# Performance work log

Hardware: AMD Instinct MI355X
Metric: run time of the kernel (lower is better)

## Reference

```python
import jax, jax.numpy as jnp
import numpy as np

C_IN = 64
C_QK = C_IN // 8  # 8
B, H, W = 8, 64, 64


def setup_inputs() -> dict:
    key = jax.random.key(0)
    ks = jax.random.split(key, 8)
    s_in = 1.0 / np.sqrt(C_IN)
    return {
        "x": jax.random.normal(ks[0], (B, C_IN, H, W), dtype=jnp.float32),
        "Wf": jax.random.normal(ks[1], (C_QK, C_IN), dtype=jnp.float32) * s_in,
        "bf": jax.random.normal(ks[2], (C_QK,), dtype=jnp.float32) * 0.01,
        "Wg": jax.random.normal(ks[3], (C_QK, C_IN), dtype=jnp.float32) * s_in,
        "bg": jax.random.normal(ks[4], (C_QK,), dtype=jnp.float32) * 0.01,
        "Wh": jax.random.normal(ks[5], (C_IN, C_IN), dtype=jnp.float32) * s_in,
        "bh": jax.random.normal(ks[6], (C_IN,), dtype=jnp.float32) * 0.01,
        "gamma": jax.random.normal(ks[7], (1,), dtype=jnp.float32) * 0.1,
    }


def reference(x, Wf, bf, Wg, bg, Wh, bh, gamma):
    Bn, C, Hn, Wn = x.shape
    N = Hn * Wn
    xf = x.reshape(Bn, C, N)  # (B, C, HW)
    # 1x1 convs == per-pixel linear projections
    fx = jnp.einsum('bcn,oc->bno', xf, Wf) + bf            # (B, HW, C/8)  (permuted query)
    gx = jnp.einsum('bcn,oc->bon', xf, Wg) + bg[:, None]   # (B, C/8, HW)
    hx = jnp.einsum('bcn,oc->bon', xf, Wh) + bh[:, None]   # (B, C,  HW)
    s_mtx = jnp.einsum('bno,bom->bnm', fx, gx)             # (B, HW, HW)
    attention = jax.nn.softmax(s_mtx, axis=-2)             # softmax over dim=-2 (rows)
    o = jnp.einsum('bcn,bnm->bcm', hx, attention)          # (B, C, HW)
    return x + gamma * o.reshape(Bn, C, Hn, Wn)
```

## Files before the change

kernel.cpp:

```cpp
#include <hip/hip_runtime.h>
#include <hip/hip_bf16.h>
#include <math.h>

#define CIN 64
#define CQK 8
#define BATCH 8
#define NPOS 4096
#define TN 128
#define NT (NPOS / TN)

typedef __attribute__((ext_vector_type(8))) short s16x8;
typedef __attribute__((ext_vector_type(4))) float f32x4;
typedef __attribute__((ext_vector_type(16))) float f32x16;

#define Z16 {0,0,0,0,0,0,0,0,0,0,0,0,0,0,0,0}

#define SCH_BIAS 1065353216.0f

__device__ inline unsigned cvt_pk_bf16(float lo, float hi) {
    unsigned r;
    asm("v_cvt_pk_bf16_f32 %0, %1, %2" : "=v"(r) : "v"(lo), "v"(hi));
    return r;
}
__device__ inline float sch_exp(float y) {
    return __builtin_bit_cast(float, (int)y);
}

__global__ __launch_bounds__(256) void proj_kernel(
    const float* __restrict__ x,
    const float* __restrict__ Wf, const float* __restrict__ bf,
    const float* __restrict__ Wg, const float* __restrict__ bg,
    const float* __restrict__ Wh, const float* __restrict__ bh,
    unsigned short* __restrict__ Kp, unsigned short* __restrict__ Qp,
    unsigned short* __restrict__ Vimg)
{
    __shared__ float xs[CIN * 34];
    __shared__ float bss[80];

    const int tid = threadIdx.x;
    const int b   = blockIdx.y;
    const int n0  = blockIdx.x * 32;

    if (tid < 80)
        bss[tid] = (tid < 8) ? bf[tid] : (tid < 16) ? bg[tid - 8] : bh[tid - 16];

    {
        const int c   = tid >> 2;
        const int seg = tid & 3;
        const float* src = x + ((size_t)(b * CIN + c)) * NPOS + n0 + seg * 8;
        float* dst = xs + c * 34 + seg * 8;
#pragma unroll
        for (int k = 0; k < 2; ++k) {
            const float4 v = *(const float4*)(src + k * 4);
            *(float2*)(dst + k * 4)     = make_float2(v.x, v.y);
            *(float2*)(dst + k * 4 + 2) = make_float2(v.z, v.w);
        }
    }

    const int l    = tid & 63;
    const int w    = tid >> 6;
    const int ng   = w >> 1;
    const int role = w & 1;
    const int lm   = l & 15;
    const int h    = l >> 4;

    auto wfrag = [&](const float* Wrow) -> s16x8 {
        const float4 a  = *(const float4*)(Wrow);
        const float4 bq = *(const float4*)(Wrow + 4);
        union { unsigned u[4]; s16x8 v; } r;
        r.u[0] = cvt_pk_bf16(a.x, a.y);
        r.u[1] = cvt_pk_bf16(a.z, a.w);
        r.u[2] = cvt_pk_bf16(bq.x, bq.y);
        r.u[3] = cvt_pk_bf16(bq.z, bq.w);
        return r.v;
    };

    s16x8 wkq0 = {0,0,0,0,0,0,0,0}, wkq1 = {0,0,0,0,0,0,0,0};
    if (role == 0) {
        const float* kqrow = (lm < 8) ? (Wf + lm * CIN) : (Wg + (lm - 8) * CIN);
        wkq0 = wfrag(kqrow + h * 8);
        wkq1 = wfrag(kqrow + h * 8 + 32);
    }
    s16x8 wv0[2], wv1[2];
#pragma unroll
    for (int vt = 0; vt < 2; ++vt) {
        const float* vr = Wh + ((role * 2 + vt) * 16 + lm) * CIN + h * 8;
        wv0[vt] = wfrag(vr);
        wv1[vt] = wfrag(vr + 32);
    }

    __syncthreads();

    union { unsigned u[4]; s16x8 v; } xf0, xf1;
#pragma unroll
    for (int e2 = 0; e2 < 4; ++e2) {
        const int c = h * 8 + e2 * 2;
        xf0.u[e2] = cvt_pk_bf16(xs[c * 34 + ng * 16 + lm],
                                xs[(c + 1) * 34 + ng * 16 + lm]);
        xf1.u[e2] = cvt_pk_bf16(xs[(c + 32) * 34 + ng * 16 + lm],
                                xs[(c + 33) * 34 + ng * 16 + lm]);
    }

    const f32x4 z = {0.f, 0.f, 0.f, 0.f};
    f32x4 va[2];
#pragma unroll
    for (int vt = 0; vt < 2; ++vt) {
        va[vt] = __builtin_amdgcn_mfma_f32_16x16x32_bf16(xf0.v, wv0[vt], z, 0, 0, 0);
        va[vt] = __builtin_amdgcn_mfma_f32_16x16x32_bf16(xf1.v, wv1[vt], va[vt], 0, 0, 0);
    }

    const float QSCALE = 1.44269504088896f * 8388608.0f;

    if (role == 0) {
        f32x4 kq = __builtin_amdgcn_mfma_f32_16x16x32_bf16(wkq0, xf0.v, z, 0, 0, 0);
        kq = __builtin_amdgcn_mfma_f32_16x16x32_bf16(wkq1, xf1.v, kq, 0, 0, 0);
        const int n = n0 + ng * 16 + lm;
        float v0 = kq[0] + bss[h * 4 + 0];
        float v1 = kq[1] + bss[h * 4 + 1];
        float v2 = kq[2] + bss[h * 4 + 2];
        float v3 = kq[3] + bss[h * 4 + 3];
        if (h >= 2) { v0 *= QSCALE; v1 *= QSCALE; v2 *= QSCALE; v3 *= QSCALE; }
        uint2 pk;
        pk.x = cvt_pk_bf16(v0, v1);
        pk.y = cvt_pk_bf16(v2, v3);
        unsigned short* dstq =
            (h < 2 ? Kp : Qp) + ((size_t)(b * NPOS + n)) * CQK + (h & 1) * 4;
        *(uint2*)dstq = pk;
    }

    {
        const int t128 = n0 >> 7;
        const int sub  = (n0 & 127) >> 5;
        unsigned short* dstB =
            Vimg + ((size_t)(b * 32 + t128)) * 8192 + (size_t)sub * 2048;
        const int jj   = (h & 1) * 2 + ng;
        const int half = h >> 1;
#pragma unroll
        for (int vt = 0; vt < 2; ++vt) {
            const int C = (role * 2 + vt) * 16 + lm;
            const float bb = bss[16 + C];
            uint2 pk;
            pk.x = cvt_pk_bf16(va[vt][0] + bb, va[vt][1] + bb);
            pk.y = cvt_pk_bf16(va[vt][2] + bb, va[vt][3] + bb);
            const int p = ((jj & 1) * 2 + (C >> 5)) * 64 + (jj >> 1) * 32 + (C & 31);
            *(uint2*)(dstB + p * 8 + half * 4) = pk;
        }
    }
}

__global__ __launch_bounds__(256, 2) void attn_kernel(
    const unsigned short* __restrict__ Kp, const unsigned short* __restrict__ Qp,
    const unsigned short* __restrict__ Vimg, const float* __restrict__ x,
    const float* __restrict__ gamma, float* __restrict__ out)
{
    __shared__ __align__(16) float smem[4 * 64 * 36 + 256];
    float* reg = smem;
    float* rsl = smem + 4 * 64 * 36;

    const int tid = threadIdx.x;
    const int l   = tid & 63;
    const int w   = tid >> 6;
    const int lc  = l & 31;
    const int h   = l >> 5;
    const int id  = blockIdx.x;
    const int b   = id & 7;
    const int m0  = (id >> 3) * 64;

    const unsigned short* Kbat = Kp + (size_t)b * NPOS * CQK;
    const char* Vbat = (const char*)(Vimg + (size_t)b * NPOS * CIN);

    s16x8 qf0 = {0,0,0,0,0,0,0,0}, qf1 = {0,0,0,0,0,0,0,0};
    if (h == 0) {
        qf0 = *(const s16x8*)(Qp + ((size_t)(b * NPOS + m0 + lc)) * CQK);
        qf1 = *(const s16x8*)(Qp + ((size_t)(b * NPOS + m0 + 32 + lc)) * CQK);
    }

    f32x16 acc00 = Z16, acc01 = Z16, acc10 = Z16, acc11 = Z16;
    f32x16 rs0 = Z16, rs1 = Z16;
    const s16x8 vones = {0x3F80, 0x3F80, 0x3F80, 0x3F80,
                         0x3F80, 0x3F80, 0x3F80, 0x3F80};
    const f32x16 bias16 = {SCH_BIAS, SCH_BIAS, SCH_BIAS, SCH_BIAS,
                           SCH_BIAS, SCH_BIAS, SCH_BIAS, SCH_BIAS,
                           SCH_BIAS, SCH_BIAS, SCH_BIAS, SCH_BIAS,
                           SCH_BIAS, SCH_BIAS, SCH_BIAS, SCH_BIAS};

    s16x8 vfA[4], vfB[4], ka0, ka1;
    f32x16 sc0, sc1;

    auto loadV = [&](s16x8* vf, int t) {
        const char* base = Vbat + (size_t)t * 16384 + w * 4096 + l * 16;
#pragma unroll
        for (int c = 0; c < 4; ++c)
            vf[c] = *(const s16x8*)(base + c * 1024);
    };
    auto loadK = [&](s16x8& kr, int t) {
        kr = *(const s16x8*)(Kbat + ((size_t)(t * TN + w * 32 + lc)) * CQK);
    };

    auto slot = [&](s16x8* vfCur, const s16x8& kaUse, s16x8& kaLd,
                    int t, int doNext) {
        if (doNext) asm volatile("s_waitcnt vmcnt(4)" ::: "memory");
        else        asm volatile("s_waitcnt vmcnt(0)" ::: "memory");
        __builtin_amdgcn_s_setprio(1);
        union { unsigned u[4]; s16x8 v; } A1, A2, B1, B2;
#pragma unroll
        for (int i = 0; i < 4; ++i) {
            A1.u[i] = cvt_pk_bf16(sch_exp(sc0[2 * i]),     sch_exp(sc0[2 * i + 1]));
            A2.u[i] = cvt_pk_bf16(sch_exp(sc0[8 + 2 * i]), sch_exp(sc0[9 + 2 * i]));
            B1.u[i] = cvt_pk_bf16(sch_exp(sc1[2 * i]),     sch_exp(sc1[2 * i + 1]));
            B2.u[i] = cvt_pk_bf16(sch_exp(sc1[8 + 2 * i]), sch_exp(sc1[9 + 2 * i]));
        }
        if (doNext) {
            sc0 = __builtin_amdgcn_mfma_f32_32x32x16_bf16(kaUse, qf0, bias16, 0, 0, 0);
            sc1 = __builtin_amdgcn_mfma_f32_32x32x16_bf16(kaUse, qf1, bias16, 0, 0, 0);
            int tl = t + 2; if (tl > NT - 1) tl = NT - 1;
            loadK(kaLd, tl);
        }
        rs0 = __builtin_amdgcn_mfma_f32_32x32x16_bf16(A1.v, vones, rs0, 0, 0, 0);
        rs0 = __builtin_amdgcn_mfma_f32_32x32x16_bf16(A2.v, vones, rs0, 0, 0, 0);
        rs1 = __builtin_amdgcn_mfma_f32_32x32x16_bf16(B1.v, vones, rs1, 0, 0, 0);
        rs1 = __builtin_amdgcn_mfma_f32_32x32x16_bf16(B2.v, vones, rs1, 0, 0, 0);
        acc00 = __builtin_amdgcn_mfma_f32_32x32x16_bf16(A1.v, vfCur[0], acc00, 0, 0, 0);
        acc00 = __builtin_amdgcn_mfma_f32_32x32x16_bf16(A2.v, vfCur[2], acc00, 0, 0, 0);
        acc01 = __builtin_amdgcn_mfma_f32_32x32x16_bf16(A1.v, vfCur[1], acc01, 0, 0, 0);
        acc01 = __builtin_amdgcn_mfma_f32_32x32x16_bf16(A2.v, vfCur[3], acc01, 0, 0, 0);
        acc10 = __builtin_amdgcn_mfma_f32_32x32x16_bf16(B1.v, vfCur[0], acc10, 0, 0, 0);
        acc10 = __builtin_amdgcn_mfma_f32_32x32x16_bf16(B2.v, vfCur[2], acc10, 0, 0, 0);
        acc11 = __builtin_amdgcn_mfma_f32_32x32x16_bf16(B1.v, vfCur[1], acc11, 0, 0, 0);
        acc11 = __builtin_amdgcn_mfma_f32_32x32x16_bf16(B2.v, vfCur[3], acc11, 0, 0, 0);
        __builtin_amdgcn_s_setprio(0);
        if (doNext) {
            int tl = t + 2; if (tl > NT - 1) tl = NT - 1;
            loadV(vfCur, tl);
        }
    };

    loadK(ka0, 0); loadV(vfA, 0);
    loadK(ka1, 1); loadV(vfB, 1);
    asm volatile("s_waitcnt vmcnt(9)" ::: "memory");
    sc0 = __builtin_amdgcn_mfma_f32_32x32x16_bf16(ka0, qf0, bias16, 0, 0, 0);
    sc1 = __builtin_amdgcn_mfma_f32_32x32x16_bf16(ka0, qf1, bias16, 0, 0, 0);

    slot(vfA, ka1, ka0, 0, 1);
#pragma unroll 1
    for (int i = 0; i < 15; ++i) {
        const int t = 1 + 2 * i;
        slot(vfB, ka0, ka1, t, 1);
        slot(vfA, ka1, ka0, t + 1, 1);
    }
    slot(vfB, ka0, ka1, 31, 0);

    if (lc == 0) {
#pragma unroll
        for (int rq = 0; rq < 4; ++rq) {
            const int mb = 8 * rq + 4 * h;
            const f32x4 r0 = {rs0[4 * rq], rs0[4 * rq + 1], rs0[4 * rq + 2], rs0[4 * rq + 3]};
            const f32x4 r1 = {rs1[4 * rq], rs1[4 * rq + 1], rs1[4 * rq + 2], rs1[4 * rq + 3]};
            *(f32x4*)(rsl + w * 64 + mb)      = r0;
            *(f32x4*)(rsl + w * 64 + 32 + mb) = r1;
        }
    }

    const float gm = gamma[0];
    auto epi = [&](const f32x16& a0, const f32x16& a1, int mOff) {
#pragma unroll
        for (int rq = 0; rq < 4; ++rq) {
            const int mb = 8 * rq + 4 * h;
            const f32x4 q0 = {a0[4 * rq], a0[4 * rq + 1], a0[4 * rq + 2], a0[4 * rq + 3]};
            const f32x4 q1 = {a1[4 * rq], a1[4 * rq + 1], a1[4 * rq + 2], a1[4 * rq + 3]};
            *(f32x4*)(reg + w * 2304 + lc * 36 + mb)        = q0;
            *(f32x4*)(reg + w * 2304 + (32 + lc) * 36 + mb) = q1;
        }
        __syncthreads();
        const int c  = tid >> 2;
        const int mq = tid & 3;
        const size_t base = ((size_t)(b * CIN + c)) * NPOS + m0 + mOff + mq * 8;
#pragma unroll
        for (int q4 = 0; q4 < 2; ++q4) {
            const float4 xv = *(const float4*)(x + base + q4 * 4);
            float4 o;
#pragma unroll
            for (int i = 0; i < 4; ++i) {
                const int ml = mq * 8 + q4 * 4 + i;
                const float rsum = (rsl[mOff + ml] + rsl[64 + mOff + ml]) +
                                   (rsl[128 + mOff + ml] + rsl[192 + mOff + ml]);
                const int oi = c * 36 + ml;
                const float os = (reg[oi] + reg[2304 + oi]) + (reg[4608 + oi] + reg[6912 + oi]);
                ((float*)&o)[i] = ((const float*)&xv)[i] + gm * os / rsum;
            }
            *(float4*)(out + base + q4 * 4) = o;
        }
        __syncthreads();
    };
    epi(acc00, acc01, 0);
    epi(acc10, acc11, 32);
}

extern "C" void kernel_launch(void* const* d_in, const int* in_sizes, int n_in,
                              void* d_out, int out_size, void* d_ws, size_t ws_size,
                              hipStream_t stream) {
    const float* x     = (const float*)d_in[0];
    const float* Wf    = (const float*)d_in[1];
    const float* bf    = (const float*)d_in[2];
    const float* Wg    = (const float*)d_in[3];
    const float* bg    = (const float*)d_in[4];
    const float* Wh    = (const float*)d_in[5];
    const float* bh    = (const float*)d_in[6];
    const float* gamma = (const float*)d_in[7];
    float* out = (float*)d_out;

    unsigned short* Kp   = (unsigned short*)d_ws;
    unsigned short* Qp   = Kp + (size_t)BATCH * NPOS * CQK;
    unsigned short* Vimg = Qp + (size_t)BATCH * NPOS * CQK;

    dim3 pgrid(NPOS / 32, BATCH);
    proj_kernel<<<pgrid, 256, 0, stream>>>(x, Wf, bf, Wg, bg, Wh, bh, Kp, Qp, Vimg);

    attn_kernel<<<dim3(BATCH * NPOS / 64), 256, 0, stream>>>(Kp, Qp, Vimg, x, gamma, out);
}
```

Baseline: 40.73 us.

## Double key tile size and compute softmax row sums with VALU instead of MFMA

Doubles the key tile to 256 positions per iteration, so each slot loads two K fragments and eight V fragments and runs two back-to-back half steps. The attention-weight column sums are now accumulated with VALU adds and one cross-half shuffle instead of four extra MFMAs against a ones vector, which cuts matrix-core work per slot. The score MFMA is now issued inside each half step rather than software-pipelined one slot ahead, so the exp conversion waits directly on its latency. The larger register buffers also raise VGPR pressure.

```diff
diff --git a/kernel.cpp b/kernel.cpp
--- a/kernel.cpp
+++ b/kernel.cpp
@@ -6,7 +6,7 @@
 #define CQK 8
 #define BATCH 8
 #define NPOS 4096
-#define TN 128
+#define TN 256
 #define NT (NPOS / TN)
 
 typedef __attribute__((ext_vector_type(8))) short s16x8;
@@ -176,89 +176,85 @@
     }
 
     f32x16 acc00 = Z16, acc01 = Z16, acc10 = Z16, acc11 = Z16;
-    f32x16 rs0 = Z16, rs1 = Z16;
-    const s16x8 vones = {0x3F80, 0x3F80, 0x3F80, 0x3F80,
-                         0x3F80, 0x3F80, 0x3F80, 0x3F80};
+    float rsum0 = 0.f, rsum1 = 0.f;
     const f32x16 bias16 = {SCH_BIAS, SCH_BIAS, SCH_BIAS, SCH_BIAS,
                            SCH_BIAS, SCH_BIAS, SCH_BIAS, SCH_BIAS,
                            SCH_BIAS, SCH_BIAS, SCH_BIAS, SCH_BIAS,
                            SCH_BIAS, SCH_BIAS, SCH_BIAS, SCH_BIAS};
 
-    s16x8 vfA[4], vfB[4], ka0, ka1;
-    f32x16 sc0, sc1;
-
-    auto loadV = [&](s16x8* vf, int t) {
-        const char* base = Vbat + (size_t)t * 16384 + w * 4096 + l * 16;
-#pragma unroll
-        for (int c = 0; c < 4; ++c)
+    s16x8 vfA[8], vfB[8], kaA[2], kaB[2];
+
+    auto loadTile = [&](s16x8* vf, s16x8* ka, int t) {
+        const char* kb = (const char*)(Kbat + ((size_t)(t * TN + w * 64 + lc)) * CQK);
+        ka[0] = *(const s16x8*)kb;
+        ka[1] = *(const s16x8*)(kb + 32 * 16);
+        const char* base = Vbat + (size_t)t * 32768 + w * 8192 + l * 16;
+#pragma unroll
+        for (int c = 0; c < 8; ++c)
             vf[c] = *(const s16x8*)(base + c * 1024);
     };
-    auto loadK = [&](s16x8& kr, int t) {
-        kr = *(const s16x8*)(Kbat + ((size_t)(t * TN + w * 32 + lc)) * CQK);
-    };
-
-    auto slot = [&](s16x8* vfCur, const s16x8& kaUse, s16x8& kaLd,
-                    int t, int doNext) {
-        if (doNext) asm volatile("s_waitcnt vmcnt(4)" ::: "memory");
-        else        asm volatile("s_waitcnt vmcnt(0)" ::: "memory");
+
+    auto half_step = [&](const s16x8& kah, const s16x8* vfh) {
+        f32x16 sc0 = __builtin_amdgcn_mfma_f32_32x32x16_bf16(kah, qf0, bias16, 0, 0, 0);
+        f32x16 sc1 = __builtin_amdgcn_mfma_f32_32x32x16_bf16(kah, qf1, bias16, 0, 0, 0);
+        float p0[16], p1[16];
+#pragma unroll
+        for (int i = 0; i < 16; ++i) {
+            p0[i] = sch_exp(sc0[i]);
+            p1[i] = sch_exp(sc1[i]);
+        }
+        union { unsigned u[4]; s16x8 v; } A1, A2, B1, B2;
+#pragma unroll
+        for (int i = 0; i < 4; ++i) {
+            A1.u[i] = cvt_pk_bf16(p0[2 * i],     p0[2 * i + 1]);
+            A2.u[i] = cvt_pk_bf16(p0[8 + 2 * i], p0[9 + 2 * i]);
+            B1.u[i] = cvt_pk_bf16(p1[2 * i],     p1[2 * i + 1]);
+            B2.u[i] = cvt_pk_bf16(p1[8 + 2 * i], p1[9 + 2 * i]);
+        }
+        rsum0 += (((p0[0] + p0[1]) + (p0[2] + p0[3])) +
+                  ((p0[4] + p0[5]) + (p0[6] + p0[7]))) +
+                 (((p0[8] + p0[9]) + (p0[10] + p0[11])) +
+                  ((p0[12] + p0[13]) + (p0[14] + p0[15])));
+        rsum1 += (((p1[0] + p1[1]) + (p1[2] + p1[3])) +
+                  ((p1[4] + p1[5]) + (p1[6] + p1[7]))) +
+                 (((p1[8] + p1[9]) + (p1[10] + p1[11])) +
+                  ((p1[12] + p1[13]) + (p1[14] + p1[15])));
+        acc00 = __builtin_amdgcn_mfma_f32_32x32x16_bf16(A1.v, vfh[0], acc00, 0, 0, 0);
+        acc00 = __builtin_amdgcn_mfma_f32_32x32x16_bf16(A2.v, vfh[2], acc00, 0, 0, 0);
+        acc01 = __builtin_amdgcn_mfma_f32_32x32x16_bf16(A1.v, vfh[1], acc01, 0, 0, 0);
+        acc01 = __builtin_amdgcn_mfma_f32_32x32x16_bf16(A2.v, vfh[3], acc01, 0, 0, 0);
+        acc10 = __builtin_amdgcn_mfma_f32_32x32x16_bf16(B1.v, vfh[0], acc10, 0, 0, 0);
+        acc10 = __builtin_amdgcn_mfma_f32_32x32x16_bf16(B2.v, vfh[2], acc10, 0, 0, 0);
+        acc11 = __builtin_amdgcn_mfma_f32_32x32x16_bf16(B1.v, vfh[1], acc11, 0, 0, 0);
+        acc11 = __builtin_amdgcn_mfma_f32_32x32x16_bf16(B2.v, vfh[3], acc11, 0, 0, 0);
+    };
+
+    auto slot = [&](s16x8* vf, s16x8* ka, int t, int drain, int pf) {
+        if (drain) asm volatile("s_waitcnt vmcnt(0)"  ::: "memory");
+        else       asm volatile("s_waitcnt vmcnt(10)" ::: "memory");
         __builtin_amdgcn_s_setprio(1);
-        union { unsigned u[4]; s16x8 v; } A1, A2, B1, B2;
-#pragma unroll
-        for (int i = 0; i < 4; ++i) {
-            A1.u[i] = cvt_pk_bf16(sch_exp(sc0[2 * i]),     sch_exp(sc0[2 * i + 1]));
-            A2.u[i] = cvt_pk_bf16(sch_exp(sc0[8 + 2 * i]), sch_exp(sc0[9 + 2 * i]));
-            B1.u[i] = cvt_pk_bf16(sch_exp(sc1[2 * i]),     sch_exp(sc1[2 * i + 1]));
-            B2.u[i] = cvt_pk_bf16(sch_exp(sc1[8 + 2 * i]), sch_exp(sc1[9 + 2 * i]));
-        }
-        if (doNext) {
-            sc0 = __builtin_amdgcn_mfma_f32_32x32x16_bf16(kaUse, qf0, bias16, 0, 0, 0);
-            sc1 = __builtin_amdgcn_mfma_f32_32x32x16_bf16(kaUse, qf1, bias16, 0, 0, 0);
-            int tl = t + 2; if (tl > NT - 1) tl = NT - 1;
-            loadK(kaLd, tl);
-        }
-        rs0 = __builtin_amdgcn_mfma_f32_32x32x16_bf16(A1.v, vones, rs0, 0, 0, 0);
-        rs0 = __builtin_amdgcn_mfma_f32_32x32x16_bf16(A2.v, vones, rs0, 0, 0, 0);
-        rs1 = __builtin_amdgcn_mfma_f32_32x32x16_bf16(B1.v, vones, rs1, 0, 0, 0);
-        rs1 = __builtin_amdgcn_mfma_f32_32x32x16_bf16(B2.v, vones, rs1, 0, 0, 0);
-        acc00 = __builtin_amdgcn_mfma_f32_32x32x16_bf16(A1.v, vfCur[0], acc00, 0, 0, 0);
-        acc00 = __builtin_amdgcn_mfma_f32_32x32x16_bf16(A2.v, vfCur[2], acc00, 0, 0, 0);
-        acc01 = __builtin_amdgcn_mfma_f32_32x32x16_bf16(A1.v, vfCur[1], acc01, 0, 0, 0);
-        acc01 = __builtin_amdgcn_mfma_f32_32x32x16_bf16(A2.v, vfCur[3], acc01, 0, 0, 0);
-        acc10 = __builtin_amdgcn_mfma_f32_32x32x16_bf16(B1.v, vfCur[0], acc10, 0, 0, 0);
-        acc10 = __builtin_amdgcn_mfma_f32_32x32x16_bf16(B2.v, vfCur[2], acc10, 0, 0, 0);
-        acc11 = __builtin_amdgcn_mfma_f32_32x32x16_bf16(B1.v, vfCur[1], acc11, 0, 0, 0);
-        acc11 = __builtin_amdgcn_mfma_f32_32x32x16_bf16(B2.v, vfCur[3], acc11, 0, 0, 0);
+        half_step(ka[0], vf);
+        half_step(ka[1], vf + 4);
         __builtin_amdgcn_s_setprio(0);
-        if (doNext) {
-            int tl = t + 2; if (tl > NT - 1) tl = NT - 1;
-            loadV(vfCur, tl);
-        }
-    };
-
-    loadK(ka0, 0); loadV(vfA, 0);
-    loadK(ka1, 1); loadV(vfB, 1);
-    asm volatile("s_waitcnt vmcnt(9)" ::: "memory");
-    sc0 = __builtin_amdgcn_mfma_f32_32x32x16_bf16(ka0, qf0, bias16, 0, 0, 0);
-    sc1 = __builtin_amdgcn_mfma_f32_32x32x16_bf16(ka0, qf1, bias16, 0, 0, 0);
-
-    slot(vfA, ka1, ka0, 0, 1);
+        if (pf) loadTile(vf, ka, t + 2);
+    };
+
+    loadTile(vfA, kaA, 0);
+    loadTile(vfB, kaB, 1);
+
 #pragma unroll 1
-    for (int i = 0; i < 15; ++i) {
-        const int t = 1 + 2 * i;
-        slot(vfB, ka0, ka1, t, 1);
-        slot(vfA, ka1, ka0, t + 1, 1);
-    }
-    slot(vfB, ka0, ka1, 31, 0);
-
-    if (lc == 0) {
-#pragma unroll
-        for (int rq = 0; rq < 4; ++rq) {
-            const int mb = 8 * rq + 4 * h;
-            const f32x4 r0 = {rs0[4 * rq], rs0[4 * rq + 1], rs0[4 * rq + 2], rs0[4 * rq + 3]};
-            const f32x4 r1 = {rs1[4 * rq], rs1[4 * rq + 1], rs1[4 * rq + 2], rs1[4 * rq + 3]};
-            *(f32x4*)(rsl + w * 64 + mb)      = r0;
-            *(f32x4*)(rsl + w * 64 + 32 + mb) = r1;
-        }
+    for (int i = 0; i < 7; ++i) {
+        slot(vfA, kaA, 2 * i,     0, 1);
+        slot(vfB, kaB, 2 * i + 1, 0, 1);
+    }
+    slot(vfA, kaA, 14, 0, 0);
+    slot(vfB, kaB, 15, 1, 0);
+
+    rsum0 += __shfl_xor(rsum0, 32, 64);
+    rsum1 += __shfl_xor(rsum1, 32, 64);
+    if (h == 0) {
+        rsl[w * 64 + lc]      = rsum0;
+        rsl[w * 64 + 32 + lc] = rsum1;
     }
 
     const float gm = gamma[0];
```

New measurement: 38.01 us. -6.7%, faster.
